# Optimization experiments

Measured on AMD Instinct MI355X. Metric: run time of the kernel, lower is better.

The kernel has to match this reference:

```python
import jax, jax.numpy as jnp
import numpy as np

NEG_SLOPE = 0.2  # PyG GATConv default negative_slope
EPS = 1e-16


def gat_conv(x, W, att_src, att_dst, bias, src, dst, heads, out_ch, concat):
    """PyG-style GATConv (eval mode, self-loops already included in src/dst).
    x: [N, F_in]; W: [heads*out_ch, F_in]; att_src/att_dst: [1, heads, out_ch]; bias: [heads*out_ch] or [out_ch].
    """
    N = x.shape[0]
    h = (x @ W.T).reshape(N, heads, out_ch)            # [N, H, C]
    a_src = (h * att_src).sum(-1)                      # [N, H]
    a_dst = (h * att_dst).sum(-1)                      # [N, H]
    alpha = jax.nn.leaky_relu(a_src[src] + a_dst[dst], NEG_SLOPE)  # [E, H]
    # segment softmax over destination nodes
    amax = jax.ops.segment_max(alpha, dst, num_segments=N)         # [N, H]
    ex = jnp.exp(alpha - amax[dst])
    denom = jax.ops.segment_sum(ex, dst, num_segments=N)           # [N, H]
    coef = ex / (denom[dst] + EPS)                                 # [E, H]
    out = jax.ops.segment_sum(h[src] * coef[:, :, None], dst, num_segments=N)  # [N, H, C]
    if concat:
        out = out.reshape(N, heads * out_ch)
    else:
        out = out.mean(axis=1)
    return out + bias


def setup_inputs() -> dict:
    key = jax.random.key(0)
    ks = jax.random.split(key, 10)
    N, F_in, H, C, OUT, E = 50000, 128, 4, 64, 2, 800000
    x = jax.random.normal(ks[0], (N, F_in), dtype=jnp.float32)
    edge_index = jax.random.randint(ks[1], (2, E), 0, N, dtype=jnp.int64)
    glorot = lambda k, shp: jax.random.normal(k, shp, dtype=jnp.float32) * jnp.sqrt(2.0 / (shp[0] + shp[-1]))
    W1 = glorot(ks[2], (H * C, F_in))
    att_src1 = glorot(ks[3], (1, H, C))
    att_dst1 = glorot(ks[4], (1, H, C))
    b1 = jnp.zeros((H * C,), dtype=jnp.float32)
    W2 = glorot(ks[5], (1 * OUT, H * C))
    att_src2 = glorot(ks[6], (1, 1, OUT))
    att_dst2 = glorot(ks[7], (1, 1, OUT))
    b2 = jnp.zeros((OUT,), dtype=jnp.float32)
    return {"x": x, "edge_index": edge_index, "W1": W1, "att_src1": att_src1,
            "att_dst1": att_dst1, "b1": b1, "W2": W2, "att_src2": att_src2,
            "att_dst2": att_dst2, "b2": b2}


def reference(x, edge_index, W1, att_src1, att_dst1, b1, W2, att_src2, att_dst2, b2):
    N = x.shape[0]
    loop = jnp.arange(N, dtype=edge_index.dtype)
    src = jnp.concatenate([edge_index[0], loop])   # add self-loops (PyG default)
    dst = jnp.concatenate([edge_index[1], loop])
    h = gat_conv(x, W1, att_src1, att_dst1, b1, src, dst, heads=4, out_ch=64, concat=True)
    h = jax.nn.relu(h)
    out = gat_conv(h, W2, att_src2, att_dst2, b2, src, dst, heads=1, out_ch=2, concat=False)
    return out
```

## Files before the change

### kernel.cpp

```cpp
#include <hip/hip_runtime.h>
#include <hip/hip_bf16.h>
#include <stdint.h>
#include <math.h>

#define NEG_SLOPE 0.2f
#define EPSV 1e-16f
#define SLOT 64
#define NBQ 128
#define NBUCKET 391
#define CAPA 32
#define EPB 8192
#define OVCAP 64
#define NW1C 16

#define KA 0.8656170245333781f
#define KB 0.5770780163555854f

typedef __attribute__((ext_vector_type(8))) short bf16x8;
typedef __attribute__((ext_vector_type(4))) float f32x4;

static __device__ __forceinline__ float b2f(unsigned short u) {
    union { float f; uint32_t i; } v; v.i = ((uint32_t)u) << 16; return v.f;
}
static __device__ __forceinline__ uint32_t qpk(float a, float b) {
    union { float f; uint32_t u; } x, y; x.f = a; y.f = b;
    return ((x.u + 0x8000u) >> 16) | ((y.u + 0x8000u) & 0xFFFF0000u);
}

__global__ __launch_bounds__(256) void prep_bin_kernel(
    const int* __restrict__ ei, int E,
    const float* __restrict__ W1,
    const float* __restrict__ b1, const float* __restrict__ W2,
    unsigned int* __restrict__ bins, unsigned short* __restrict__ counts,
    unsigned int* __restrict__ gov, unsigned int* __restrict__ govcnt,
    unsigned short* __restrict__ w1p,
    float* __restrict__ b1p, float* __restrict__ w2p0, float* __restrict__ w2p1,
    unsigned short* __restrict__ h1, float4* __restrict__ a_src1v,
    float4* __restrict__ h2pk,
    int N, int nblk_binA)
{
    const int b = blockIdx.x, t = threadIdx.x;

    if (b < nblk_binA) {
        __shared__ unsigned int binS[NBUCKET * CAPA];
        __shared__ unsigned int binC[NBUCKET];
        __shared__ unsigned int ovn;
        const int blk = b;

        for (int i = t; i < NBUCKET; i += 256) binC[i] = 0;
        if (t == 0) ovn = 0;
        __syncthreads();

        const int e_base = blk * EPB;
        for (int i = 0; i < EPB / 256; ++i) {
            int e = e_base + i * 256 + t;
            if (e < E) {
                int s = ei[e], d = ei[E + e];
                int bk = d >> 7;
                unsigned int w = (unsigned int)s | ((unsigned int)(d & 127) << 16)
                               | ((unsigned int)bk << 23);
                unsigned int r = atomicAdd(&binC[bk], 1u);
                if (r < CAPA) binS[bk * CAPA + r] = w;
                else {
                    unsigned int o = atomicAdd(&ovn, 1u);
                    if (o < OVCAP) gov[blk * OVCAP + o] = w;
                }
            }
        }
        __syncthreads();

        for (int wdx = t; wdx < NBUCKET * CAPA; wdx += 256) {
            int bk = wdx >> 5, sl = wdx & 31;
            bins[((size_t)bk * nblk_binA + blk) * CAPA + sl] = binS[wdx];
        }
        for (int i = t; i < NBUCKET; i += 256) {
            unsigned int c = binC[i];
            counts[(size_t)i * nblk_binA + blk] = (unsigned short)(c < CAPA ? c : CAPA);
        }
        if (t == 0) govcnt[blk] = (ovn < OVCAP ? ovn : OVCAP);
    } else if (b < nblk_binA + NW1C) {
        int idx = (b - nblk_binA) * 256 + t;
        int c = idx >> 4, oct = idx & 15;
        int ct = c >> 4, l15 = c & 15;
        int kk = oct >> 2, quad = oct & 3;
        const float* sp = W1 + (size_t)c * 128 + oct * 8;
        float4 u0 = *(const float4*)(sp);
        float4 u1 = *(const float4*)(sp + 4);
        uint4 w;
        w.x = qpk(u0.x, u0.y); w.y = qpk(u0.z, u0.w);
        w.z = qpk(u1.x, u1.y); w.w = qpk(u1.z, u1.w);
        *(uint4*)(w1p + (size_t)(((kk * 16 + ct) * 4 + quad) * 128 + l15 * 8)) = w;
    } else {
        int cp = t;
        int c = (cp & 15) * 16 + (cp >> 4);
        b1p[cp]  = b1[c];
        w2p0[cp] = W2[c];
        w2p1[cp] = W2[256 + c];
        if (t < 32)
            ((uint4*)(h1 + (size_t)N * 256))[t] = make_uint4(0, 0, 0, 0);
        else if (t == 32)
            a_src1v[N] = make_float4(-1e4f, -1e4f, -1e4f, -1e4f);
        else if (t == 33)
            h2pk[N] = make_float4(0.f, 0.f, -1e4f, 0.f);
    }
}

__global__ __launch_bounds__(256, 3) void gemm_csr_kernel(
    const float* __restrict__ x,
    const unsigned short* __restrict__ w1p,
    const float* __restrict__ att_src1, const float* __restrict__ att_dst1,
    unsigned short* __restrict__ h1,
    float4* __restrict__ a_src1v, float4* __restrict__ a_dst1v,
    const unsigned int* __restrict__ bins, const unsigned short* __restrict__ counts,
    const unsigned int* __restrict__ gov, const unsigned int* __restrict__ govcnt,
    int* __restrict__ deg, unsigned short* __restrict__ csr16,
    int N, int nblk_gemm, int nblk_binA)
{
    const int t = threadIdx.x;
    __shared__ unsigned short lcsr[NBQ * SLOT];
    __shared__ unsigned int ldeg[NBQ];

    if (blockIdx.x < nblk_gemm) {
        const int wv = t >> 6, lane = t & 63;
        const int l15 = lane & 15, quad = lane >> 4;
        const int m0 = blockIdx.x * 64 + wv * 16;

        union { bf16x8 v; uint32_t u[4]; } A[4];
        {
            int m = m0 + l15;
            int mr = m < N ? m : N - 1;
            const float* ap = x + (size_t)mr * 128 + quad * 8;
            #pragma unroll
            for (int kk = 0; kk < 4; ++kk) {
                float4 u0 = *(const float4*)(ap + kk * 32);
                float4 u1 = *(const float4*)(ap + kk * 32 + 4);
                A[kk].u[0] = qpk(u0.x, u0.y);
                A[kk].u[1] = qpk(u0.z, u0.w);
                A[kk].u[2] = qpk(u1.x, u1.y);
                A[kk].u[3] = qpk(u1.z, u1.w);
            }
        }

        f32x4 acc[16];
        #pragma unroll
        for (int ct = 0; ct < 16; ++ct) acc[ct] = (f32x4){0.f, 0.f, 0.f, 0.f};

        const size_t bbase = (size_t)quad * 128 + l15 * 8;
        #pragma unroll
        for (int kk = 0; kk < 4; ++kk) {
            #pragma unroll
            for (int ct = 0; ct < 16; ++ct) {
                bf16x8 Bv = *(const bf16x8*)(w1p + (size_t)(kk * 16 + ct) * 512 + bbase);
                acc[ct] = __builtin_amdgcn_mfma_f32_16x16x32_bf16(A[kk].v, Bv, acc[ct], 0, 0, 0);
            }
        }

        #pragma unroll
        for (int r = 0; r < 4; ++r) {
            int m = m0 + quad * 4 + r;
            if (m < N) {
                uint32_t u[8];
                #pragma unroll
                for (int j = 0; j < 8; ++j)
                    u[j] = qpk(acc[2 * j][r], acc[2 * j + 1][r]);
                uint4* hp = (uint4*)(h1 + (size_t)m * 256 + l15 * 16);
                hp[0] = make_uint4(u[0], u[1], u[2], u[3]);
                hp[1] = make_uint4(u[4], u[5], u[6], u[7]);
            }
        }

        float as_l[16], ad_l[16];
        #pragma unroll
        for (int ct = 0; ct < 16; ++ct) {
            as_l[ct] = att_src1[ct * 16 + l15];
            ad_l[ct] = att_dst1[ct * 16 + l15];
        }
        #pragma unroll
        for (int r = 0; r < 4; ++r) {
            float ps[4] = {0.f, 0.f, 0.f, 0.f};
            float pd[4] = {0.f, 0.f, 0.f, 0.f};
            #pragma unroll
            for (int ct = 0; ct < 16; ++ct) {
                ps[ct >> 2] += acc[ct][r] * as_l[ct];
                pd[ct >> 2] += acc[ct][r] * ad_l[ct];
            }
            #pragma unroll
            for (int off = 1; off < 16; off <<= 1) {
                #pragma unroll
                for (int hh = 0; hh < 4; ++hh) {
                    ps[hh] += __shfl_xor(ps[hh], off);
                    pd[hh] += __shfl_xor(pd[hh], off);
                }
            }
            int m = m0 + quad * 4 + r;
            if (l15 == 0 && m < N) {
                a_src1v[m] = make_float4(ps[0], ps[1], ps[2], ps[3]);
                a_dst1v[m] = make_float4(pd[0], pd[1], pd[2], pd[3]);
            }
        }
    } else {
        const int b = blockIdx.x - nblk_gemm;
        const int base = b * NBQ;

        const unsigned int pad2 = ((unsigned int)N << 16) | (unsigned int)N;
        unsigned int* lc32 = (unsigned int*)lcsr;
        for (int i = t; i < NBQ * SLOT / 2; i += 256) lc32[i] = pad2;
        __syncthreads();
        for (int i = t; i < NBQ; i += 256) {
            ldeg[i] = 1;
            lcsr[i << 6] = (unsigned short)(base + i);
        }
        __syncthreads();

        if (t < 2 * nblk_binA) {
            int cell = t >> 1;
            int c = counts[(size_t)b * nblk_binA + cell];
            const unsigned int* cp = bins + ((size_t)b * nblk_binA + cell) * CAPA;
            for (int r = (t & 1); r < c; r += 2) {
                unsigned int w = cp[r];
                int dl = (w >> 16) & 127;
                unsigned int rank = atomicAdd(&ldeg[dl], 1u);
                if (rank < SLOT) lcsr[(dl << 6) + rank] = (unsigned short)(w & 0xFFFF);
            }
        }
        for (int idx = t; idx < nblk_binA * OVCAP; idx += 256) {
            int blk = idx >> 6, sl = idx & (OVCAP - 1);
            if (sl < (int)govcnt[blk]) {
                unsigned int w = gov[idx];
                if ((int)(w >> 23) == b) {
                    int dl = (w >> 16) & 127;
                    unsigned int rank = atomicAdd(&ldeg[dl], 1u);
                    if (rank < SLOT) lcsr[(dl << 6) + rank] = (unsigned short)(w & 0xFFFF);
                }
            }
        }
        __syncthreads();

        const int nn = min(NBQ, N - base);
        uint4* dst = (uint4*)(csr16 + (size_t)base * SLOT);
        const uint4* src = (const uint4*)lcsr;
        for (int i = t; i < nn * 8; i += 256) dst[i] = src[i];
        for (int i = t; i < nn; i += 256) deg[base + i] = (int)ldeg[i];
    }
}

__global__ __launch_bounds__(256) void agg1_layer2_kernel(
    const int* __restrict__ deg, const unsigned short* __restrict__ csr16,
    const float* __restrict__ a_src1, const float* __restrict__ a_dst1,
    const unsigned short* __restrict__ h1,
    const float* __restrict__ b1p,
    const float* __restrict__ w2p0, const float* __restrict__ w2p1,
    const float* __restrict__ as2, const float* __restrict__ ad2,
    float4* __restrict__ h2pk, int N)
{
    const int wv = threadIdx.x >> 6, lane = threadIdx.x & 63;
    const int half = lane >> 5, ll = lane & 31;
    const int n = blockIdx.x * 4 + wv;
    if (n >= N) return;
    const int h0 = (ll & 1) * 2;
    const unsigned short* cs = csr16 + (size_t)n * SLOT;
    const int dn = min(deg[n], 57);
    const float2 adh = *(const float2*)(a_dst1 + (size_t)n * 4 + h0);

    const int iters = (dn + 1) >> 1;

    const unsigned llo = (unsigned)ll * 16u;
    const unsigned ho  = (unsigned)h0 * 4u;
    const char* h1b = (const char*)h1;
    const char* asb = (const char*)a_src1;

    float acc[8] = {0.f, 0.f, 0.f, 0.f, 0.f, 0.f, 0.f, 0.f};
    float den0 = 0.f, den1 = 0.f;

    auto consume = [&](float2 av, uint4 r) {
        float a0 = av.x + adh.x, a1 = av.y + adh.y;
        float e0 = exp2f(fmaf(KB, fabsf(a0), KA * a0));
        float e1 = exp2f(fmaf(KB, fabsf(a1), KA * a1));
        den0 += e0; den1 += e1;
        union { unsigned u; float f; } lo, hi;
        lo.u = r.x << 16; hi.u = r.x & 0xFFFF0000u;
        acc[0] = fmaf(e0, lo.f, acc[0]); acc[1] = fmaf(e0, hi.f, acc[1]);
        lo.u = r.y << 16; hi.u = r.y & 0xFFFF0000u;
        acc[2] = fmaf(e0, lo.f, acc[2]); acc[3] = fmaf(e0, hi.f, acc[3]);
        lo.u = r.z << 16; hi.u = r.z & 0xFFFF0000u;
        acc[4] = fmaf(e1, lo.f, acc[4]); acc[5] = fmaf(e1, hi.f, acc[5]);
        lo.u = r.w << 16; hi.u = r.w & 0xFFFF0000u;
        acc[6] = fmaf(e1, lo.f, acc[6]); acc[7] = fmaf(e1, hi.f, acc[7]);
    };

    int ia = half, ib = half + 2, ic = half + 4, id = half + 6;
    unsigned s0 = cs[ia], s1 = cs[ib], s2 = cs[ic], s3 = cs[id];
    uint4  rA = *(const uint4*)(h1b + s0 * 512u + llo);
    float2 aA = *(const float2*)(asb + s0 * 16u + ho);
    uint4  rB = *(const uint4*)(h1b + s1 * 512u + llo);
    float2 aB = *(const float2*)(asb + s1 * 16u + ho);
    uint4  rC = *(const uint4*)(h1b + s2 * 512u + llo);
    float2 aC = *(const float2*)(asb + s2 * 16u + ho);
    uint4  rD = *(const uint4*)(h1b + s3 * 512u + llo);
    float2 aD = *(const float2*)(asb + s3 * 16u + ho);

    int k = 0;
    for (; k + 4 < iters; k += 4) {
        unsigned n0 = cs[ia + 8], n1 = cs[ib + 8], n2 = cs[ic + 8], n3 = cs[id + 8];
        consume(aA, rA);
        rA = *(const uint4*)(h1b + n0 * 512u + llo);
        aA = *(const float2*)(asb + n0 * 16u + ho);
        consume(aB, rB);
        rB = *(const uint4*)(h1b + n1 * 512u + llo);
        aB = *(const float2*)(asb + n1 * 16u + ho);
        consume(aC, rC);
        rC = *(const uint4*)(h1b + n2 * 512u + llo);
        aC = *(const float2*)(asb + n2 * 16u + ho);
        consume(aD, rD);
        rD = *(const uint4*)(h1b + n3 * 512u + llo);
        aD = *(const float2*)(asb + n3 * 16u + ho);
        ia += 8; ib += 8; ic += 8; id += 8;
    }
    const int rem = iters - k;
    consume(aA, rA);
    if (rem > 1) consume(aB, rB);
    if (rem > 2) consume(aC, rC);
    if (rem > 3) consume(aD, rD);

    #pragma unroll
    for (int kq = 0; kq < 8; ++kq) acc[kq] += __shfl_xor(acc[kq], 32);
    den0 += __shfl_xor(den0, 32);
    den1 += __shfl_xor(den1, 32);

    const float inv0 = 1.f / (den0 + EPSV);
    const float inv1 = 1.f / (den1 + EPSV);
    const int c0 = ll * 8;
    float4 ba = *(const float4*)(b1p + c0);
    float4 bb = *(const float4*)(b1p + c0 + 4);
    float v[8];
    v[0] = acc[0] * inv0 + ba.x; v[1] = acc[1] * inv0 + ba.y;
    v[2] = acc[2] * inv0 + ba.z; v[3] = acc[3] * inv0 + ba.w;
    v[4] = acc[4] * inv1 + bb.x; v[5] = acc[5] * inv1 + bb.y;
    v[6] = acc[6] * inv1 + bb.z; v[7] = acc[7] * inv1 + bb.w;
    #pragma unroll
    for (int kq = 0; kq < 8; ++kq) v[kq] = v[kq] > 0.f ? v[kq] : 0.f;

    float4 w0a = *(const float4*)(w2p0 + c0);
    float4 w0b = *(const float4*)(w2p0 + c0 + 4);
    float4 w1a = *(const float4*)(w2p1 + c0);
    float4 w1b = *(const float4*)(w2p1 + c0 + 4);
    float p0 = v[0]*w0a.x + v[1]*w0a.y + v[2]*w0a.z + v[3]*w0a.w
             + v[4]*w0b.x + v[5]*w0b.y + v[6]*w0b.z + v[7]*w0b.w;
    float p1 = v[0]*w1a.x + v[1]*w1a.y + v[2]*w1a.z + v[3]*w1a.w
             + v[4]*w1b.x + v[5]*w1b.y + v[6]*w1b.z + v[7]*w1b.w;
    #pragma unroll
    for (int off = 16; off; off >>= 1) {
        p0 += __shfl_xor(p0, off);
        p1 += __shfl_xor(p1, off);
    }
    if (lane == 0) {
        h2pk[n] = make_float4(p0, p1,
                              p0 * as2[0] + p1 * as2[1],
                              p0 * ad2[0] + p1 * ad2[1]);
    }
}

__global__ __launch_bounds__(256) void aggregate2_csr_kernel(
    const int* __restrict__ deg, const unsigned short* __restrict__ csr16,
    const float4* __restrict__ h2pk,
    const float* __restrict__ b2, float* __restrict__ out, int N)
{
    const int wv = threadIdx.x >> 6, lane = threadIdx.x & 63;
    const int g = lane >> 4, q = lane & 15;
    const int n = blockIdx.x * 16 + wv * 4 + g;
    if (n >= N) return;
    const unsigned short* cs = csr16 + (size_t)n * SLOT;
    const int dn = min(deg[n], SLOT);
    float ad = h2pk[n].w;
    float den = 0.f, num0 = 0.f, num1 = 0.f;
    const char* hb = (const char*)h2pk;
    const int trip = (dn + 15) >> 4;
    for (int k = 0; k < trip; ++k) {
        unsigned s = cs[q + (k << 4)];
        float4 hq = *(const float4*)(hb + s * 16u);
        float aa = hq.z + ad;
        float ex = exp2f(fmaf(KB, fabsf(aa), KA * aa));
        den += ex;
        num0 = fmaf(ex, hq.x, num0);
        num1 = fmaf(ex, hq.y, num1);
    }
    #pragma unroll
    for (int off = 8; off; off >>= 1) {
        den  += __shfl_xor(den, off);
        num0 += __shfl_xor(num0, off);
        num1 += __shfl_xor(num1, off);
    }
    if (q == 0) {
        float inv = 1.f / (den + EPSV);
        out[(size_t)n * 2]     = num0 * inv + b2[0];
        out[(size_t)n * 2 + 1] = num1 * inv + b2[1];
    }
}

extern "C" void kernel_launch(void* const* d_in, const int* in_sizes, int n_in,
                              void* d_out, int out_size, void* d_ws, size_t ws_size,
                              hipStream_t stream)
{
    const float* x   = (const float*)d_in[0];
    const int*   ei  = (const int*)d_in[1];
    const float* W1  = (const float*)d_in[2];
    const float* as1 = (const float*)d_in[3];
    const float* ad1 = (const float*)d_in[4];
    const float* b1  = (const float*)d_in[5];
    const float* W2  = (const float*)d_in[6];
    const float* as2 = (const float*)d_in[7];
    const float* ad2 = (const float*)d_in[8];
    const float* b2p = (const float*)d_in[9];

    const int N  = in_sizes[0] / 128;
    const int E  = in_sizes[1] / 2;

    const int NB        = (N + NBQ - 1) / NBQ;
    const int nblk_gemm = (N + 63) / 64;
    const int nblk_binA = (E + EPB - 1) / EPB;

    char* ws = (char*)d_ws;
    size_t off = 0;
    auto alloc = [&](size_t bytes) -> char* {
        char* p = ws + off;
        off = (off + bytes + 255) & ~(size_t)255;
        return p;
    };
    unsigned short* h1 = (unsigned short*)alloc((size_t)(N + 1) * 256 * 2);
    float* a_src1  = (float*)alloc((size_t)(N + 1) * 4 * 4);
    float* a_dst1  = (float*)alloc((size_t)N * 4 * 4);
    float4* h2pk   = (float4*)alloc((size_t)(N + 1) * 16);
    float* b1pp    = (float*)alloc((size_t)256 * 4);
    float* w2p0    = (float*)alloc((size_t)256 * 4);
    float* w2p1    = (float*)alloc((size_t)256 * 4);
    int*   deg     = (int*)alloc((size_t)N * 4);
    unsigned short* csr16 = (unsigned short*)alloc((size_t)N * SLOT * 2);
    unsigned int*   bins  = (unsigned int*)alloc((size_t)NB * nblk_binA * CAPA * 4);
    unsigned short* cnts  = (unsigned short*)alloc((size_t)NB * nblk_binA * 2);
    unsigned int*   gov   = (unsigned int*)alloc((size_t)nblk_binA * OVCAP * 4);
    unsigned int*   govcnt= (unsigned int*)alloc((size_t)nblk_binA * 4);
    unsigned short* w1pb  = (unsigned short*)alloc((size_t)256 * 128 * 2);

    prep_bin_kernel<<<nblk_binA + NW1C + 1, 256, 0, stream>>>(
        ei, E, W1, b1, W2,
        bins, cnts, gov, govcnt, w1pb, b1pp, w2p0, w2p1,
        h1, (float4*)a_src1, h2pk, N, nblk_binA);
    gemm_csr_kernel<<<nblk_gemm + NB, 256, 0, stream>>>(
        x, w1pb, as1, ad1, h1, (float4*)a_src1, (float4*)a_dst1,
        bins, cnts, gov, govcnt, deg, csr16, N, nblk_gemm, nblk_binA);
    agg1_layer2_kernel<<<(N + 3) / 4, 256, 0, stream>>>(
        deg, csr16, a_src1, a_dst1, h1,
        b1pp, w2p0, w2p1, as2, ad2, h2pk, N);
    aggregate2_csr_kernel<<<(N + 15) / 16, 256, 0, stream>>>(
        deg, csr16, h2pk, b2p, (float*)d_out, N);
}
```

Measured before the change: 193.9 us.

## Make layer-1 aggregation persistent with prefetch of next node's CSR header

The agg1_layer2 kernel becomes a grid-stride persistent loop over nodes with the grid capped at 2048 blocks. While a node's first neighbour rows load, it prefetches the next node's degree, first 8 CSR entries (one uint4) and a_dst values. The first four neighbour indices now come out of that vector load, so the first gathers no longer wait on a separate dependent load. This targets per-wave launch and dependent-load latency at the cost of less parallelism per launch and possible load imbalance.

```diff
diff --git a/kernel.cpp b/kernel.cpp
--- a/kernel.cpp
+++ b/kernel.cpp
@@ -255,109 +255,124 @@
 {
     const int wv = threadIdx.x >> 6, lane = threadIdx.x & 63;
     const int half = lane >> 5, ll = lane & 31;
-    const int n = blockIdx.x * 4 + wv;
-    if (n >= N) return;
+    const int NW = gridDim.x * 4;
     const int h0 = (ll & 1) * 2;
-    const unsigned short* cs = csr16 + (size_t)n * SLOT;
-    const int dn = min(deg[n], 57);
-    const float2 adh = *(const float2*)(a_dst1 + (size_t)n * 4 + h0);
-
-    const int iters = (dn + 1) >> 1;
-
+    const int hsh = half * 16;
     const unsigned llo = (unsigned)ll * 16u;
     const unsigned ho  = (unsigned)h0 * 4u;
     const char* h1b = (const char*)h1;
     const char* asb = (const char*)a_src1;
 
-    float acc[8] = {0.f, 0.f, 0.f, 0.f, 0.f, 0.f, 0.f, 0.f};
-    float den0 = 0.f, den1 = 0.f;
-
-    auto consume = [&](float2 av, uint4 r) {
-        float a0 = av.x + adh.x, a1 = av.y + adh.y;
-        float e0 = exp2f(fmaf(KB, fabsf(a0), KA * a0));
-        float e1 = exp2f(fmaf(KB, fabsf(a1), KA * a1));
-        den0 += e0; den1 += e1;
-        union { unsigned u; float f; } lo, hi;
-        lo.u = r.x << 16; hi.u = r.x & 0xFFFF0000u;
-        acc[0] = fmaf(e0, lo.f, acc[0]); acc[1] = fmaf(e0, hi.f, acc[1]);
-        lo.u = r.y << 16; hi.u = r.y & 0xFFFF0000u;
-        acc[2] = fmaf(e0, lo.f, acc[2]); acc[3] = fmaf(e0, hi.f, acc[3]);
-        lo.u = r.z << 16; hi.u = r.z & 0xFFFF0000u;
-        acc[4] = fmaf(e1, lo.f, acc[4]); acc[5] = fmaf(e1, hi.f, acc[5]);
-        lo.u = r.w << 16; hi.u = r.w & 0xFFFF0000u;
-        acc[6] = fmaf(e1, lo.f, acc[6]); acc[7] = fmaf(e1, hi.f, acc[7]);
-    };
-
-    int ia = half, ib = half + 2, ic = half + 4, id = half + 6;
-    unsigned s0 = cs[ia], s1 = cs[ib], s2 = cs[ic], s3 = cs[id];
-    uint4  rA = *(const uint4*)(h1b + s0 * 512u + llo);
-    float2 aA = *(const float2*)(asb + s0 * 16u + ho);
-    uint4  rB = *(const uint4*)(h1b + s1 * 512u + llo);
-    float2 aB = *(const float2*)(asb + s1 * 16u + ho);
-    uint4  rC = *(const uint4*)(h1b + s2 * 512u + llo);
-    float2 aC = *(const float2*)(asb + s2 * 16u + ho);
-    uint4  rD = *(const uint4*)(h1b + s3 * 512u + llo);
-    float2 aD = *(const float2*)(asb + s3 * 16u + ho);
-
-    int k = 0;
-    for (; k + 4 < iters; k += 4) {
-        unsigned n0 = cs[ia + 8], n1 = cs[ib + 8], n2 = cs[ic + 8], n3 = cs[id + 8];
+    int n = blockIdx.x * 4 + wv;
+    if (n >= N) return;
+
+    int dn_p = deg[n];
+    uint4 cs8_p = *(const uint4*)(csr16 + (size_t)n * SLOT);
+    float2 adh_p = *(const float2*)(a_dst1 + (size_t)n * 4 + h0);
+
+    #define LDH(s) (*(const uint4*)(h1b + (unsigned)(s) * 512u + llo))
+    #define LDA(s) (*(const float2*)(asb + (unsigned)(s) * 16u + ho))
+
+    while (true) {
+        const int dn = min(dn_p, 57);
+        const uint4 cs8 = cs8_p;
+        const float2 adh = adh_p;
+        const unsigned short* cs = csr16 + (size_t)n * SLOT;
+        const int n_next = n + NW;
+        const int iters = (dn + 1) >> 1;
+
+        unsigned s0 = (cs8.x >> hsh) & 0xFFFFu;
+        unsigned s1 = (cs8.y >> hsh) & 0xFFFFu;
+        unsigned s2 = (cs8.z >> hsh) & 0xFFFFu;
+        unsigned s3 = (cs8.w >> hsh) & 0xFFFFu;
+        uint4  rA = LDH(s0); float2 aA = LDA(s0);
+        uint4  rB = LDH(s1); float2 aB = LDA(s1);
+        uint4  rC = LDH(s2); float2 aC = LDA(s2);
+        uint4  rD = LDH(s3); float2 aD = LDA(s3);
+
+        if (n_next < N) {
+            dn_p  = deg[n_next];
+            cs8_p = *(const uint4*)(csr16 + (size_t)n_next * SLOT);
+            adh_p = *(const float2*)(a_dst1 + (size_t)n_next * 4 + h0);
+        }
+
+        float acc[8] = {0.f, 0.f, 0.f, 0.f, 0.f, 0.f, 0.f, 0.f};
+        float den0 = 0.f, den1 = 0.f;
+
+        auto consume = [&](float2 av, uint4 r) {
+            float a0 = av.x + adh.x, a1 = av.y + adh.y;
+            float e0 = exp2f(fmaf(KB, fabsf(a0), KA * a0));
+            float e1 = exp2f(fmaf(KB, fabsf(a1), KA * a1));
+            den0 += e0; den1 += e1;
+            union { unsigned u; float f; } lo, hi;
+            lo.u = r.x << 16; hi.u = r.x & 0xFFFF0000u;
+            acc[0] = fmaf(e0, lo.f, acc[0]); acc[1] = fmaf(e0, hi.f, acc[1]);
+            lo.u = r.y << 16; hi.u = r.y & 0xFFFF0000u;
+            acc[2] = fmaf(e0, lo.f, acc[2]); acc[3] = fmaf(e0, hi.f, acc[3]);
+            lo.u = r.z << 16; hi.u = r.z & 0xFFFF0000u;
+            acc[4] = fmaf(e1, lo.f, acc[4]); acc[5] = fmaf(e1, hi.f, acc[5]);
+            lo.u = r.w << 16; hi.u = r.w & 0xFFFF0000u;
+            acc[6] = fmaf(e1, lo.f, acc[6]); acc[7] = fmaf(e1, hi.f, acc[7]);
+        };
+
+        int ia = half, ib = half + 2, ic = half + 4, id = half + 6;
+        int k = 0;
+        for (; k + 4 < iters; k += 4) {
+            unsigned n0 = cs[ia + 8], n1 = cs[ib + 8], n2 = cs[ic + 8], n3 = cs[id + 8];
+            consume(aA, rA); rA = LDH(n0); aA = LDA(n0);
+            consume(aB, rB); rB = LDH(n1); aB = LDA(n1);
+            consume(aC, rC); rC = LDH(n2); aC = LDA(n2);
+            consume(aD, rD); rD = LDH(n3); aD = LDA(n3);
+            ia += 8; ib += 8; ic += 8; id += 8;
+        }
+        const int rem = iters - k;
         consume(aA, rA);
-        rA = *(const uint4*)(h1b + n0 * 512u + llo);
-        aA = *(const float2*)(asb + n0 * 16u + ho);
-        consume(aB, rB);
-        rB = *(const uint4*)(h1b + n1 * 512u + llo);
-        aB = *(const float2*)(asb + n1 * 16u + ho);
-        consume(aC, rC);
-        rC = *(const uint4*)(h1b + n2 * 512u + llo);
-        aC = *(const float2*)(asb + n2 * 16u + ho);
-        consume(aD, rD);
-        rD = *(const uint4*)(h1b + n3 * 512u + llo);
-        aD = *(const float2*)(asb + n3 * 16u + ho);
-        ia += 8; ib += 8; ic += 8; id += 8;
-    }
-    const int rem = iters - k;
-    consume(aA, rA);
-    if (rem > 1) consume(aB, rB);
-    if (rem > 2) consume(aC, rC);
-    if (rem > 3) consume(aD, rD);
-
-    #pragma unroll
-    for (int kq = 0; kq < 8; ++kq) acc[kq] += __shfl_xor(acc[kq], 32);
-    den0 += __shfl_xor(den0, 32);
-    den1 += __shfl_xor(den1, 32);
-
-    const float inv0 = 1.f / (den0 + EPSV);
-    const float inv1 = 1.f / (den1 + EPSV);
-    const int c0 = ll * 8;
-    float4 ba = *(const float4*)(b1p + c0);
-    float4 bb = *(const float4*)(b1p + c0 + 4);
-    float v[8];
-    v[0] = acc[0] * inv0 + ba.x; v[1] = acc[1] * inv0 + ba.y;
-    v[2] = acc[2] * inv0 + ba.z; v[3] = acc[3] * inv0 + ba.w;
-    v[4] = acc[4] * inv1 + bb.x; v[5] = acc[5] * inv1 + bb.y;
-    v[6] = acc[6] * inv1 + bb.z; v[7] = acc[7] * inv1 + bb.w;
-    #pragma unroll
-    for (int kq = 0; kq < 8; ++kq) v[kq] = v[kq] > 0.f ? v[kq] : 0.f;
-
-    float4 w0a = *(const float4*)(w2p0 + c0);
-    float4 w0b = *(const float4*)(w2p0 + c0 + 4);
-    float4 w1a = *(const float4*)(w2p1 + c0);
-    float4 w1b = *(const float4*)(w2p1 + c0 + 4);
-    float p0 = v[0]*w0a.x + v[1]*w0a.y + v[2]*w0a.z + v[3]*w0a.w
-             + v[4]*w0b.x + v[5]*w0b.y + v[6]*w0b.z + v[7]*w0b.w;
-    float p1 = v[0]*w1a.x + v[1]*w1a.y + v[2]*w1a.z + v[3]*w1a.w
-             + v[4]*w1b.x + v[5]*w1b.y + v[6]*w1b.z + v[7]*w1b.w;
-    #pragma unroll
-    for (int off = 16; off; off >>= 1) {
-        p0 += __shfl_xor(p0, off);
-        p1 += __shfl_xor(p1, off);
-    }
-    if (lane == 0) {
-        h2pk[n] = make_float4(p0, p1,
-                              p0 * as2[0] + p1 * as2[1],
-                              p0 * ad2[0] + p1 * ad2[1]);
-    }
+        if (rem > 1) consume(aB, rB);
+        if (rem > 2) consume(aC, rC);
+        if (rem > 3) consume(aD, rD);
+
+        #pragma unroll
+        for (int kq = 0; kq < 8; ++kq) acc[kq] += __shfl_xor(acc[kq], 32);
+        den0 += __shfl_xor(den0, 32);
+        den1 += __shfl_xor(den1, 32);
+
+        const float inv0 = 1.f / (den0 + EPSV);
+        const float inv1 = 1.f / (den1 + EPSV);
+        const int c0 = ll * 8;
+        float4 ba = *(const float4*)(b1p + c0);
+        float4 bb = *(const float4*)(b1p + c0 + 4);
+        float v[8];
+        v[0] = acc[0] * inv0 + ba.x; v[1] = acc[1] * inv0 + ba.y;
+        v[2] = acc[2] * inv0 + ba.z; v[3] = acc[3] * inv0 + ba.w;
+        v[4] = acc[4] * inv1 + bb.x; v[5] = acc[5] * inv1 + bb.y;
+        v[6] = acc[6] * inv1 + bb.z; v[7] = acc[7] * inv1 + bb.w;
+        #pragma unroll
+        for (int kq = 0; kq < 8; ++kq) v[kq] = v[kq] > 0.f ? v[kq] : 0.f;
+
+        float4 w0a = *(const float4*)(w2p0 + c0);
+        float4 w0b = *(const float4*)(w2p0 + c0 + 4);
+        float4 w1a = *(const float4*)(w2p1 + c0);
+        float4 w1b = *(const float4*)(w2p1 + c0 + 4);
+        float p0 = v[0]*w0a.x + v[1]*w0a.y + v[2]*w0a.z + v[3]*w0a.w
+                 + v[4]*w0b.x + v[5]*w0b.y + v[6]*w0b.z + v[7]*w0b.w;
+        float p1 = v[0]*w1a.x + v[1]*w1a.y + v[2]*w1a.z + v[3]*w1a.w
+                 + v[4]*w1b.x + v[5]*w1b.y + v[6]*w1b.z + v[7]*w1b.w;
+        #pragma unroll
+        for (int off = 16; off; off >>= 1) {
+            p0 += __shfl_xor(p0, off);
+            p1 += __shfl_xor(p1, off);
+        }
+        if (lane == 0) {
+            h2pk[n] = make_float4(p0, p1,
+                                  p0 * as2[0] + p1 * as2[1],
+                                  p0 * ad2[0] + p1 * ad2[1]);
+        }
+
+        if (n_next >= N) break;
+        n = n_next;
+    }
+    #undef LDH
+    #undef LDA
 }
 
 __global__ __launch_bounds__(256) void aggregate2_csr_kernel(
@@ -418,6 +433,8 @@
     const int NB        = (N + NBQ - 1) / NBQ;
     const int nblk_gemm = (N + 63) / 64;
     const int nblk_binA = (E + EPB - 1) / EPB;
+    int nblk_agg1 = (N + 3) / 4;
+    if (nblk_agg1 > 2048) nblk_agg1 = 2048;
 
     char* ws = (char*)d_ws;
     size_t off = 0;
@@ -448,7 +465,7 @@
     gemm_csr_kernel<<<nblk_gemm + NB, 256, 0, stream>>>(
         x, w1pb, as1, ad1, h1, (float4*)a_src1, (float4*)a_dst1,
         bins, cnts, gov, govcnt, deg, csr16, N, nblk_gemm, nblk_binA);
-    agg1_layer2_kernel<<<(N + 3) / 4, 256, 0, stream>>>(
+    agg1_layer2_kernel<<<nblk_agg1, 256, 0, stream>>>(
         deg, csr16, a_src1, a_dst1, h1,
         b1pp, w2p0, w2p1, as2, ad2, h2pk, N);
     aggregate2_csr_kernel<<<(N + 15) / 16, 256, 0, stream>>>(
```

After: 196.6 us. No clear change (+1.4%).
